# Performance work log

Measured on AMD Instinct MI355X. Metric: run time of the kernel, lower is better.

## Reference

```python
import jax, jax.numpy as jnp
import numpy as np

N_TABLES = 26
VOCAB = 100000
M_SPA = 64
B = 8192
N_DENSE = 13
N_FEAT = N_TABLES + 1  # 27 features entering interaction
LI, LJ = np.tril_indices(N_FEAT, k=-1)  # strictly-lower pairs, matches torch li/lj order


def setup_inputs() -> dict:
    key = jax.random.key(0)
    ks = jax.random.split(key, 16)
    dense_x = jax.random.normal(ks[0], (B, N_DENSE), dtype=jnp.float32)
    lS_i = jax.random.randint(ks[1], (N_TABLES, B), 0, VOCAB, dtype=jnp.int64)
    # one index per bag -> offsets are arange(B) for every table
    lS_o = jnp.tile(jnp.arange(B, dtype=jnp.int64)[None, :], (N_TABLES, 1))
    # embedding tables, uniform(-sqrt(1/n), sqrt(1/n)) as in create_emb
    s = np.sqrt(1.0 / VOCAB)
    Wemb = jax.random.uniform(ks[2], (N_TABLES, VOCAB, M_SPA), dtype=jnp.float32, minval=-s, maxval=s)

    def mk_lin(k, n, m):
        k1, k2 = jax.random.split(k)
        W = jax.random.normal(k1, (m, n), dtype=jnp.float32) * np.sqrt(2.0 / (m + n))
        b = jax.random.normal(k2, (m,), dtype=jnp.float32) * np.sqrt(1.0 / m)
        return W, b

    bW0, bb0 = mk_lin(ks[3], 13, 512)
    bW1, bb1 = mk_lin(ks[4], 512, 256)
    bW2, bb2 = mk_lin(ks[5], 256, 64)
    tW0, tb0 = mk_lin(ks[6], 415, 512)
    tW1, tb1 = mk_lin(ks[7], 512, 256)
    tW2, tb2 = mk_lin(ks[8], 256, 1)
    return dict(dense_x=dense_x, lS_i=lS_i, lS_o=lS_o, Wemb=Wemb,
                bW0=bW0, bb0=bb0, bW1=bW1, bb1=bb1, bW2=bW2, bb2=bb2,
                tW0=tW0, tb0=tb0, tW1=tW1, tb1=tb1, tW2=tW2, tb2=tb2)


def reference(dense_x, lS_i, lS_o, Wemb,
              bW0, bb0, bW1, bb1, bW2, bb2,
              tW0, tb0, tW1, tb1, tW2, tb2):
    # bottom MLP (all ReLU, sigmoid_bot=-1)
    x = jax.nn.relu(dense_x @ bW0.T + bb0)
    x = jax.nn.relu(x @ bW1.T + bb1)
    x = jax.nn.relu(x @ bW2.T + bb2)  # [B, 64]
    # multi-table EmbeddingBag(sum) with one index per bag == plain gather
    ly = jax.vmap(lambda W, idx: W[idx])(Wemb, lS_i)  # [26, B, 64]
    # dot interaction
    T = jnp.concatenate([x[:, None, :], jnp.transpose(ly, (1, 0, 2))], axis=1)  # [B, 27, 64]
    Z = jnp.einsum('bnd,bmd->bnm', T, T)  # [B, 27, 27]
    Zflat = Z[:, LI, LJ]  # [B, 351]
    R = jnp.concatenate([x, Zflat], axis=1)  # [B, 415]
    # top MLP: ReLU, ReLU, Sigmoid (sigmoid_top=2)
    z = jax.nn.relu(R @ tW0.T + tb0)
    z = jax.nn.relu(z @ tW1.T + tb1)
    p = jax.nn.sigmoid(z @ tW2.T + tb2)  # [B, 1]
    # loss_threshold = 0.0 -> no clamp
    return p
```

## Files before the change

kernel.cpp:

```cpp
#include <hip/hip_runtime.h>
#include <hip/hip_bf16.h>


typedef _Float16 f16x8 __attribute__((ext_vector_type(8)));
typedef float f32x4 __attribute__((ext_vector_type(4)));

__device__ __forceinline__ f16x8 cvt8(float4 a, float4 b) {
  f16x8 f;
  f[0] = (_Float16)a.x; f[1] = (_Float16)a.y;
  f[2] = (_Float16)a.z; f[3] = (_Float16)a.w;
  f[4] = (_Float16)b.x; f[5] = (_Float16)b.y;
  f[6] = (_Float16)b.z; f[7] = (_Float16)b.w;
  return f;
}

__device__ __forceinline__ void tile_store_frag(
    _Float16* __restrict__ dst, const float* __restrict__ src,
    int i, int Ksrc, int NKK)
{
  int e = i & 7;
  int lane = (i >> 3) & 63;
  int rc = lane & 15, g = lane >> 4;
  int q = i >> 9;
  int kk = q % NKK;
  int j = q / NKK;
  int c = j * 16 + rc;
  int k = kk * 32 + g * 8 + e;
  dst[i] = (_Float16)((k < Ksrc) ? src[(size_t)c * Ksrc + k] : 0.0f);
}

__global__ __launch_bounds__(256) void prep_kernel(
    const float* __restrict__ bW0, const float* __restrict__ bW1,
    const float* __restrict__ bW2, const float* __restrict__ tW0,
    const float* __restrict__ tW1,
    _Float16* __restrict__ w0, _Float16* __restrict__ w1,
    _Float16* __restrict__ w2, _Float16* __restrict__ t0,
    _Float16* __restrict__ t1)
{
  int i = blockIdx.x * 256 + threadIdx.x;
  if (i < 16384)  { tile_store_frag(w0, bW0, i, 13, 1);   return; }
  i -= 16384;
  if (i < 131072) { tile_store_frag(w1, bW1, i, 512, 16); return; }
  i -= 131072;
  if (i < 16384)  { tile_store_frag(w2, bW2, i, 256, 8);  return; }
  i -= 16384;
  if (i < 229376) { tile_store_frag(t0, tW0, i, 415, 14); return; }
  i -= 229376;
  if (i < 131072) { tile_store_frag(t1, tW1, i, 512, 16); return; }
}

__global__ __launch_bounds__(1024, 1) void fused_kernel(
    const float* __restrict__ dense, const int* __restrict__ lSi,
    const float* __restrict__ Wemb,
    const _Float16* __restrict__ w0, const float* __restrict__ bb0,
    const _Float16* __restrict__ w1, const float* __restrict__ bb1,
    const _Float16* __restrict__ w2, const float* __restrict__ bb2,
    const _Float16* __restrict__ t0w, const float* __restrict__ tb0,
    const _Float16* __restrict__ t1w, const float* __restrict__ tb1,
    const float* __restrict__ tW2, const float* __restrict__ tb2,
    float* __restrict__ out)
{
  __shared__ __align__(16) char regA[32768];
  __shared__ __align__(16) char regB[28672];
  _Float16* x1s = (_Float16*)regA;
  _Float16* x3s = (_Float16*)regA;
  _Float16* z1s = (_Float16*)regA;
  float*    dns = (float*)regB;
  _Float16* x2s = (_Float16*)regB;
  _Float16* Rs  = (_Float16*)regB;
  float*    psm = (float*)regB;

  const int t = threadIdx.x;
  const int lane = t & 63, wv = t >> 6;
  const int rc = lane & 15, g = lane >> 4;
  const int ko = g * 8;
  const int sw = (rc & 7) << 3;
  const int b0 = blockIdx.x * 32;

  if (t < 416) {
    int r = t / 13, c = t - r * 13;
    dns[r * 16 + c] = dense[(size_t)b0 * 13 + t];
  } else if (t < 512) {
    int q = t - 416;
    int r = q / 3, c = 13 + (q - r * 3);
    dns[r * 16 + c] = 0.0f;
  }
  __syncthreads();

  {
    f16x8 af[2];
#pragma unroll
    for (int rt = 0; rt < 2; ++rt) {
      f16x8 a = {};
      if (g < 2) {
        const float* s = &dns[(rt * 16 + rc) * 16 + ko];
        a = cvt8(*(const float4*)s, *(const float4*)(s + 4));
      }
      af[rt] = a;
    }
    f32x4 acc[2][2] = {};
#pragma unroll
    for (int j = 0; j < 2; ++j) {
      const int jb = wv * 2 + j;
      f16x8 wf = *(const f16x8*)&w0[(size_t)(jb * 64 + lane) * 8];
#pragma unroll
      for (int rt = 0; rt < 2; ++rt)
        acc[rt][j] = __builtin_amdgcn_mfma_f32_16x16x32_f16(af[rt], wf, acc[rt][j], 0, 0, 0);
    }
#pragma unroll
    for (int j = 0; j < 2; ++j) {
      const int col = wv * 32 + j * 16 + rc;
      const float bs = bb0[col];
#pragma unroll
      for (int rt = 0; rt < 2; ++rt)
#pragma unroll
        for (int r = 0; r < 4; ++r) {
          int row = rt * 16 + g * 4 + r;
          float v = fmaxf(acc[rt][j][r] + bs, 0.0f);
          x1s[row * 512 + (col ^ ((row & 7) << 3))] = (_Float16)v;
        }
    }
  }
  __syncthreads();

  {
    f32x4 acc[2] = {};
#pragma unroll
    for (int kk = 0; kk < 16; ++kk) {
      f16x8 af[2];
#pragma unroll
      for (int rt = 0; rt < 2; ++rt)
        af[rt] = *(const f16x8*)&x1s[(rt * 16 + rc) * 512 + ((kk * 32 + ko) ^ sw)];
      f16x8 wf = *(const f16x8*)&w1[(size_t)((wv * 16 + kk) * 64 + lane) * 8];
#pragma unroll
      for (int rt = 0; rt < 2; ++rt)
        acc[rt] = __builtin_amdgcn_mfma_f32_16x16x32_f16(af[rt], wf, acc[rt], 0, 0, 0);
    }
    const int col = wv * 16 + rc;
    const float bs = bb1[col];
#pragma unroll
    for (int rt = 0; rt < 2; ++rt)
#pragma unroll
      for (int r = 0; r < 4; ++r) {
        int row = rt * 16 + g * 4 + r;
        float v = fmaxf(acc[rt][r] + bs, 0.0f);
        x2s[row * 256 + (col ^ ((row & 7) << 3))] = (_Float16)v;
      }
  }
  __syncthreads();

  if (wv < 8) {
    const int rt = wv & 1;
    const int cb = (wv >> 1) * 16;
    f32x4 acc = {};
#pragma unroll
    for (int kk = 0; kk < 8; ++kk) {
      f16x8 af = *(const f16x8*)&x2s[(rt * 16 + rc) * 256 + ((kk * 32 + ko) ^ sw)];
      f16x8 wf = *(const f16x8*)&w2[(size_t)(((cb >> 4) * 8 + kk) * 64 + lane) * 8];
      acc = __builtin_amdgcn_mfma_f32_16x16x32_f16(af, wf, acc, 0, 0, 0);
    }
    const int col = cb + rc;
    const float bs = bb2[col];
#pragma unroll
    for (int r = 0; r < 4; ++r) {
      int row = rt * 16 + g * 4 + r;
      float v = fmaxf(acc[r] + bs, 0.0f);
      x3s[row * 64 + col] = (_Float16)v;
    }
  }
  __syncthreads();

  {
    int e_idx[2][2];
#pragma unroll
    for (int i = 0; i < 2; ++i) {
      const int b = b0 + wv * 2 + i;
#pragma unroll
      for (int rt = 0; rt < 2; ++rt) {
        const int gr = rt * 16 + rc;
        e_idx[i][rt] = (gr >= 1 && gr <= 26) ? lSi[(size_t)(gr - 1) * 8192 + b] : 0;
      }
    }
#pragma unroll
    for (int i = 0; i < 2; ++i) {
      const int bl = wv * 2 + i;
      const int swr = (bl & 7) << 3;
      f16x8 frag[2][2];
#pragma unroll
      for (int rt = 0; rt < 2; ++rt) {
        const int gr = rt * 16 + rc;
        if (gr == 0) {
          frag[rt][0] = *(const f16x8*)&x3s[bl * 64 + ko];
          frag[rt][1] = *(const f16x8*)&x3s[bl * 64 + 32 + ko];
        } else if (gr <= 26) {
          const float* src = Wemb + ((size_t)(gr - 1) * 100000 + (size_t)e_idx[i][rt]) * 64;
#pragma unroll
          for (int kh = 0; kh < 2; ++kh) {
            const float* s = src + kh * 32 + ko;
            frag[rt][kh] = cvt8(*(const float4*)s, *(const float4*)(s + 4));
          }
        } else {
          f16x8 z = {};
          frag[rt][0] = z; frag[rt][1] = z;
        }
      }
      f32x4 z00 = {}, z10 = {}, z11 = {};
#pragma unroll
      for (int kh = 0; kh < 2; ++kh) {
        z00 = __builtin_amdgcn_mfma_f32_16x16x32_f16(frag[0][kh], frag[0][kh], z00, 0, 0, 0);
        z10 = __builtin_amdgcn_mfma_f32_16x16x32_f16(frag[1][kh], frag[0][kh], z10, 0, 0, 0);
        z11 = __builtin_amdgcn_mfma_f32_16x16x32_f16(frag[1][kh], frag[1][kh], z11, 0, 0, 0);
      }
      Rs[bl * 448 + (lane ^ swr)] = x3s[bl * 64 + lane];
      if (lane < 33) Rs[bl * 448 + ((415 + lane) ^ swr)] = (_Float16)0.0f;
      const int col = lane & 15;
      const int rr0 = (lane >> 4) * 4;
#pragma unroll
      for (int r = 0; r < 4; ++r) {
        const int i0 = rr0 + r;
        if (i0 > col) {
          int p = 64 + i0 * (i0 - 1) / 2 + col;
          Rs[bl * 448 + (p ^ swr)] = (_Float16)z00[r];
        }
        const int i1 = 16 + rr0 + r;
        if (i1 < 27) {
          int p = 64 + i1 * (i1 - 1) / 2 + col;
          Rs[bl * 448 + (p ^ swr)] = (_Float16)z10[r];
          const int j1 = 16 + col;
          if (i1 > j1) {
            int q = 64 + i1 * (i1 - 1) / 2 + j1;
            Rs[bl * 448 + (q ^ swr)] = (_Float16)z11[r];
          }
        }
      }
    }
  }
  __syncthreads();

  {
    f32x4 acc[2][2] = {};
#pragma unroll
    for (int kk = 0; kk < 14; ++kk) {
      f16x8 af[2];
#pragma unroll
      for (int rt = 0; rt < 2; ++rt)
        af[rt] = *(const f16x8*)&Rs[(rt * 16 + rc) * 448 + ((kk * 32 + ko) ^ sw)];
#pragma unroll
      for (int j = 0; j < 2; ++j) {
        const int jb = wv * 2 + j;
        f16x8 wf = *(const f16x8*)&t0w[(size_t)((jb * 14 + kk) * 64 + lane) * 8];
#pragma unroll
        for (int rt = 0; rt < 2; ++rt)
          acc[rt][j] = __builtin_amdgcn_mfma_f32_16x16x32_f16(af[rt], wf, acc[rt][j], 0, 0, 0);
      }
    }
#pragma unroll
    for (int j = 0; j < 2; ++j) {
      const int col = wv * 32 + j * 16 + rc;
      const float bs = tb0[col];
#pragma unroll
      for (int rt = 0; rt < 2; ++rt)
#pragma unroll
        for (int r = 0; r < 4; ++r) {
          int row = rt * 16 + g * 4 + r;
          float v = fmaxf(acc[rt][j][r] + bs, 0.0f);
          z1s[row * 512 + (col ^ ((row & 7) << 3))] = (_Float16)v;
        }
    }
  }
  __syncthreads();

  {
    f32x4 acc[2] = {};
#pragma unroll
    for (int kk = 0; kk < 16; ++kk) {
      f16x8 af[2];
#pragma unroll
      for (int rt = 0; rt < 2; ++rt)
        af[rt] = *(const f16x8*)&z1s[(rt * 16 + rc) * 512 + ((kk * 32 + ko) ^ sw)];
      f16x8 wf = *(const f16x8*)&t1w[(size_t)((wv * 16 + kk) * 64 + lane) * 8];
#pragma unroll
      for (int rt = 0; rt < 2; ++rt)
        acc[rt] = __builtin_amdgcn_mfma_f32_16x16x32_f16(af[rt], wf, acc[rt], 0, 0, 0);
    }
    const int col = wv * 16 + rc;
    const float bz = tb1[col];
    const float wz = tW2[col];
    float pd[2][4];
#pragma unroll
    for (int rt = 0; rt < 2; ++rt)
#pragma unroll
      for (int r = 0; r < 4; ++r)
        pd[rt][r] = fmaxf(acc[rt][r] + bz, 0.0f) * wz;
    __syncthreads();
#pragma unroll
    for (int rt = 0; rt < 2; ++rt)
#pragma unroll
      for (int r = 0; r < 4; ++r) {
        float v = pd[rt][r];
        v += __shfl_xor(v, 1, 64);
        v += __shfl_xor(v, 2, 64);
        v += __shfl_xor(v, 4, 64);
        v += __shfl_xor(v, 8, 64);
        if (rc == 0) psm[wv * 32 + rt * 16 + g * 4 + r] = v;
      }
  }
  __syncthreads();
  if (t < 32) {
    float s = tb2[0];
#pragma unroll
    for (int w = 0; w < 16; ++w) s += psm[w * 32 + t];
    out[b0 + t] = 1.0f / (1.0f + expf(-s));
  }
}

extern "C" void kernel_launch(void* const* d_in, const int* in_sizes, int n_in,
                              void* d_out, int out_size, void* d_ws, size_t ws_size,
                              hipStream_t stream)
{
  (void)in_sizes; (void)n_in; (void)out_size; (void)ws_size;
  const float* dense = (const float*)d_in[0];
  const int*   lSi   = (const int*)d_in[1];
  const float* Wemb  = (const float*)d_in[3];
  const float* bW0 = (const float*)d_in[4];  const float* bb0 = (const float*)d_in[5];
  const float* bW1 = (const float*)d_in[6];  const float* bb1 = (const float*)d_in[7];
  const float* bW2 = (const float*)d_in[8];  const float* bb2 = (const float*)d_in[9];
  const float* tW0 = (const float*)d_in[10]; const float* tb0 = (const float*)d_in[11];
  const float* tW1 = (const float*)d_in[12]; const float* tb1 = (const float*)d_in[13];
  const float* tW2 = (const float*)d_in[14]; const float* tb2 = (const float*)d_in[15];
  float* out = (float*)d_out;

  char* ws = (char*)d_ws;
  size_t off = 0;
  auto alloc = [&](size_t bytes) -> void* {
    void* p = ws + off;
    off += (bytes + 255) & ~(size_t)255;
    return p;
  };
  _Float16* w0 = (_Float16*)alloc((size_t)16384 * 2);
  _Float16* w1 = (_Float16*)alloc((size_t)131072 * 2);
  _Float16* w2 = (_Float16*)alloc((size_t)16384 * 2);
  _Float16* t0 = (_Float16*)alloc((size_t)229376 * 2);
  _Float16* t1 = (_Float16*)alloc((size_t)131072 * 2);

  prep_kernel<<<2048, 256, 0, stream>>>(bW0, bW1, bW2, tW0, tW1,
                                        w0, w1, w2, t0, t1);
  fused_kernel<<<256, 1024, 0, stream>>>(dense, lSi, Wemb,
                                         w0, bb0, w1, bb1, w2, bb2,
                                         t0, tb0, t1, tb1, tW2, tb2, out);
}
```

Before: 36.84 us.

## Vectorize weight prep, stage embedding indices in LDS, prefetch embedding rows early

The weight-prep kernel now has each thread convert and store one 8-element fp16 fragment, so it launches 256 blocks instead of 2048. In the fused kernel, the embedding indices for the block are loaded into shared memory during the dense-input staging phase, using otherwise idle threads. All embedding-row gathers for both batch rows are then issued together before any conversion or MFMA, to overlap the random-access latency. This uses more registers for the prefetched float4 values and adds a small shared-memory buffer.

```diff
diff --git a/kernel.cpp b/kernel.cpp
--- a/kernel.cpp
+++ b/kernel.cpp
@@ -14,19 +14,20 @@
   return f;
 }
 
-__device__ __forceinline__ void tile_store_frag(
+__device__ __forceinline__ void frag_store(
     _Float16* __restrict__ dst, const float* __restrict__ src,
-    int i, int Ksrc, int NKK)
+    int fl, int Ksrc, int NKK)
 {
-  int e = i & 7;
-  int lane = (i >> 3) & 63;
-  int rc = lane & 15, g = lane >> 4;
-  int q = i >> 9;
-  int kk = q % NKK;
-  int j = q / NKK;
-  int c = j * 16 + rc;
-  int k = kk * 32 + g * 8 + e;
-  dst[i] = (_Float16)((k < Ksrc) ? src[(size_t)c * Ksrc + k] : 0.0f);
+  int lane = fl & 63, q = fl >> 6;
+  int kk = q % NKK, j = q / NKK;
+  int c = j * 16 + (lane & 15);
+  int kb = kk * 32 + (lane >> 4) * 8;
+  const float* s = src + (size_t)c * Ksrc + kb;
+  f16x8 o;
+#pragma unroll
+  for (int e = 0; e < 8; ++e)
+    o[e] = (_Float16)((kb + e < Ksrc) ? s[e] : 0.0f);
+  *(f16x8*)&dst[(size_t)fl * 8] = o;
 }
 
 __global__ __launch_bounds__(256) void prep_kernel(
@@ -37,16 +38,16 @@
     _Float16* __restrict__ w2, _Float16* __restrict__ t0,
     _Float16* __restrict__ t1)
 {
-  int i = blockIdx.x * 256 + threadIdx.x;
-  if (i < 16384)  { tile_store_frag(w0, bW0, i, 13, 1);   return; }
-  i -= 16384;
-  if (i < 131072) { tile_store_frag(w1, bW1, i, 512, 16); return; }
-  i -= 131072;
-  if (i < 16384)  { tile_store_frag(w2, bW2, i, 256, 8);  return; }
-  i -= 16384;
-  if (i < 229376) { tile_store_frag(t0, tW0, i, 415, 14); return; }
-  i -= 229376;
-  if (i < 131072) { tile_store_frag(t1, tW1, i, 512, 16); return; }
+  int f = blockIdx.x * 256 + threadIdx.x;
+  if (f < 2048)  { frag_store(w0, bW0, f, 13, 1);  return; }
+  f -= 2048;
+  if (f < 16384) { frag_store(w1, bW1, f, 512, 16); return; }
+  f -= 16384;
+  if (f < 2048)  { frag_store(w2, bW2, f, 256, 8);  return; }
+  f -= 2048;
+  if (f < 28672) { frag_store(t0, tW0, f, 415, 14); return; }
+  f -= 28672;
+  if (f < 16384) { frag_store(t1, tW1, f, 512, 16); return; }
 }
 
 __global__ __launch_bounds__(1024, 1) void fused_kernel(
@@ -62,6 +63,7 @@
 {
   __shared__ __align__(16) char regA[32768];
   __shared__ __align__(16) char regB[28672];
+  __shared__ int idxs[26 * 32];
   _Float16* x1s = (_Float16*)regA;
   _Float16* x3s = (_Float16*)regA;
   _Float16* z1s = (_Float16*)regA;
@@ -84,6 +86,13 @@
     int q = t - 416;
     int r = q / 3, c = 13 + (q - r * 3);
     dns[r * 16 + c] = 0.0f;
+  } else {
+    int u = t - 512;
+    idxs[u] = (int)lSi[(size_t)(u >> 5) * 8192 + b0 + (u & 31)];
+  }
+  if (t < 320) {
+    int u = 512 + t;
+    idxs[u] = (int)lSi[(size_t)(u >> 5) * 8192 + b0 + (u & 31)];
   }
   __syncthreads();
 
@@ -171,16 +180,31 @@
   __syncthreads();
 
   {
-    int e_idx[2][2];
+    const float* srcs[2][2];
 #pragma unroll
     for (int i = 0; i < 2; ++i) {
-      const int b = b0 + wv * 2 + i;
+      const int bl = wv * 2 + i;
 #pragma unroll
       for (int rt = 0; rt < 2; ++rt) {
         const int gr = rt * 16 + rc;
-        e_idx[i][rt] = (gr >= 1 && gr <= 26) ? lSi[(size_t)(gr - 1) * 8192 + b] : 0;
-      }
-    }
+        const bool live = (gr >= 1 && gr <= 26);
+        const int tb = live ? gr - 1 : 0;
+        const int idx = live ? idxs[tb * 32 + bl] : 0;
+        srcs[i][rt] = Wemb + ((size_t)tb * 100000 + (size_t)idx) * 64;
+      }
+    }
+    float4 pf[2][2][2][2];
+#pragma unroll
+    for (int i = 0; i < 2; ++i)
+#pragma unroll
+      for (int rt = 0; rt < 2; ++rt)
+#pragma unroll
+        for (int kh = 0; kh < 2; ++kh) {
+          const float* s = srcs[i][rt] + kh * 32 + ko;
+          pf[i][rt][kh][0] = *(const float4*)s;
+          pf[i][rt][kh][1] = *(const float4*)(s + 4);
+        }
+
 #pragma unroll
     for (int i = 0; i < 2; ++i) {
       const int bl = wv * 2 + i;
@@ -193,12 +217,8 @@
           frag[rt][0] = *(const f16x8*)&x3s[bl * 64 + ko];
           frag[rt][1] = *(const f16x8*)&x3s[bl * 64 + 32 + ko];
         } else if (gr <= 26) {
-          const float* src = Wemb + ((size_t)(gr - 1) * 100000 + (size_t)e_idx[i][rt]) * 64;
-#pragma unroll
-          for (int kh = 0; kh < 2; ++kh) {
-            const float* s = src + kh * 32 + ko;
-            frag[rt][kh] = cvt8(*(const float4*)s, *(const float4*)(s + 4));
-          }
+          frag[rt][0] = cvt8(pf[i][rt][0][0], pf[i][rt][0][1]);
+          frag[rt][1] = cvt8(pf[i][rt][1][0], pf[i][rt][1][1]);
         } else {
           f16x8 z = {};
           frag[rt][0] = z; frag[rt][1] = z;
@@ -343,8 +363,8 @@
   _Float16* t0 = (_Float16*)alloc((size_t)229376 * 2);
   _Float16* t1 = (_Float16*)alloc((size_t)131072 * 2);
 
-  prep_kernel<<<2048, 256, 0, stream>>>(bW0, bW1, bW2, tW0, tW1,
-                                        w0, w1, w2, t0, t1);
+  prep_kernel<<<256, 256, 0, stream>>>(bW0, bW1, bW2, tW0, tW1,
+                                       w0, w1, w2, t0, t1);
   fused_kernel<<<256, 1024, 0, stream>>>(dense, lSi, Wemb,
                                          w0, bb0, w1, bb1, w2, bb2,
                                          t0, tb0, t1, tb1, tW2, tb2, out);
```

New measurement: 39.72 us. 7.8% more time.
